# Kernel tuning notes

Measured on AMD Instinct MI355X. Metric: run time of the kernel, lower is better.

Reference implementation:

```python
import jax, jax.numpy as jnp
import numpy as np

B, NS, NN = 1024, 1, 64
F = 128            # feat_dim = edge_dim = time_dim = pos_dim
DM = 4 * F         # model_dim = 512
H, DK = 2, 256     # n_head, d_k = d_v = model_dim // n_head
LN_EPS = 1e-5


def setup_inputs() -> dict:
    key = jax.random.key(0)
    ks = jax.random.split(key, 20)
    s = 0.02
    inp = {
        'src':   jax.random.normal(ks[0], (B, NS, F), jnp.float32),
        'src_t': jax.random.normal(ks[1], (B, NS, F), jnp.float32),
        'src_p': jax.random.normal(ks[2], (B, NS, F), jnp.float32),
        'seq':   jax.random.normal(ks[3], (B, NN, F), jnp.float32),
        'seq_t': jax.random.normal(ks[4], (B, NN, F), jnp.float32),
        'seq_e': jax.random.normal(ks[5], (B, NN, F), jnp.float32),
        'seq_p': jax.random.normal(ks[6], (B, NN, F), jnp.float32),
        'mask':  jax.random.randint(ks[7], (B, NS, NN), 0, 2).astype(bool),
        # MapBasedMultiHeadAttention params
        'wq': jax.random.normal(ks[8], (H * DK, DM), jnp.float32) * s,
        'wk': jax.random.normal(ks[9], (H * DK, DM), jnp.float32) * s,
        'wv': jax.random.normal(ks[10], (H * DK, DM), jnp.float32) * s,
        'wm': jax.random.normal(ks[11], (2 * DK,), jnp.float32) * s,   # weight_map: Linear(2*d_k, 1, bias=False)
        'fc_w': jax.random.normal(ks[12], (DM, H * DK), jnp.float32) * s,
        'fc_b': jnp.zeros((DM,), jnp.float32),
        'ln_g': jnp.ones((DM,), jnp.float32),
        'ln_b': jnp.zeros((DM,), jnp.float32),
        # MergeLayer(model_dim, feat_dim, feat_dim, feat_dim)
        'm1_w': jax.random.normal(ks[13], (F, DM + F), jnp.float32) * s,
        'm1_b': jnp.zeros((F,), jnp.float32),
        'm2_w': jax.random.normal(ks[14], (F, F), jnp.float32) * s,
        'm2_b': jnp.zeros((F,), jnp.float32),
    }
    return inp


def reference(src, src_t, src_p, seq, seq_t, seq_e, seq_p, mask,
              wq, wk, wv, wm, fc_w, fc_b, ln_g, ln_b, m1_w, m1_b, m2_w, m2_b):
    b, ns, f = src.shape
    nn = seq.shape[1]
    src_e = jnp.zeros((b, ns, f), src.dtype)  # edge feats of sources are zero
    q = jnp.concatenate([src, src_e, src_t, src_p], axis=-1)   # [B,NS,DM]
    k = jnp.concatenate([seq, seq_e, seq_t, seq_p], axis=-1)   # [B,NN,DM]

    # per-head projections: weight [H*DK, DM] -> [H, DK, DM]
    qh = jnp.einsum('bsd,hed->bshe', q, wq.reshape(H, DK, DM))  # [B,NS,H,DK]
    kh = jnp.einsum('bnd,hed->bnhe', k, wk.reshape(H, DK, DM))  # [B,NN,H,DK]
    vh = jnp.einsum('bnd,hed->bnhe', k, wv.reshape(H, DK, DM))  # [B,NN,H,DK]

    # weight_map(Linear over concat([q,k])) == q @ wm[:DK] + k @ wm[DK:]
    score_q = jnp.einsum('bshe,e->bhs', qh, wm[:DK])            # [B,H,NS]
    score_k = jnp.einsum('bnhe,e->bhn', kh, wm[DK:])            # [B,H,NN]
    attn = score_q[..., None] + score_k[:, :, None, :]          # [B,H,NS,NN]
    attn = jnp.where(mask[:, None, :, :], jnp.float32(-1e10), attn)
    attn = jax.nn.softmax(attn, axis=-1)

    out = jnp.einsum('bhsn,bnhe->bshe', attn, vh).reshape(b, ns, H * DK)
    out = jnp.einsum('bsd,ed->bse', out, fc_w) + fc_b           # fc
    out = jnp.where(out >= 0, out, 0.2 * out)                   # LeakyReLU(0.2)
    out = out + q                                               # residual
    mu = out.mean(axis=-1, keepdims=True)
    var = out.var(axis=-1, keepdims=True)
    out = (out - mu) / jnp.sqrt(var + LN_EPS) * ln_g + ln_b     # LayerNorm

    # MergeLayer (non_linear=True)
    x = jnp.concatenate([out, src], axis=-1)                    # [B,NS,DM+F]
    hdn = jax.nn.relu(jnp.einsum('bsd,ed->bse', x, m1_w) + m1_b)
    z = jnp.einsum('bsd,ed->bse', hdn, m2_w) + m2_b             # [B,NS,F]

    # attn in original layout: [n_head*B, len_q, len_k]
    attn_flat = attn.transpose(1, 0, 2, 3).reshape(H * b, ns, nn)
    return (z, attn_flat)
```

## Files before the change

kernel.cpp:

```cpp
#include <hip/hip_runtime.h>
#include <hip/hip_bf16.h>
#include <stdint.h>

#define B_   1024
#define NN_  64
#define F_   128
#define DM_  512
#define DK_  256

typedef unsigned short u16;
using f32x4  = __attribute__((ext_vector_type(4))) float;
using bf16x8 = __attribute__((ext_vector_type(8))) short;

__device__ __forceinline__ uint32_t f2bf(float x) {
  uint32_t u = __builtin_bit_cast(uint32_t, x);
  return (u + 0x7fffu + ((u >> 16) & 1u)) >> 16;
}
__device__ __forceinline__ float bf2f(uint32_t us) {
  return __builtin_bit_cast(float, us << 16);
}
__device__ __forceinline__ void split_pack(float x, float y, uint32_t& hp, uint32_t& lp) {
  uint32_t hx = f2bf(x), hy = f2bf(y);
  uint32_t lx = f2bf(x - bf2f(hx)), ly = f2bf(y - bf2f(hy));
  hp = hx | (hy << 16);
  lp = lx | (ly << 16);
}
__device__ __forceinline__ void split1(float x, u16& h, u16& l) {
  uint32_t hx = f2bf(x);
  h = (u16)hx;
  l = (u16)f2bf(x - bf2f(hx));
}

__global__ __launch_bounds__(256) void k_prep(
    const float* __restrict__ wv, const float* __restrict__ fc_w,
    const float* __restrict__ m1_w, const float* __restrict__ m2_w,
    const float* __restrict__ wk, const float* __restrict__ wm,
    u16* __restrict__ fc_hi, u16* __restrict__ fc_lo,
    u16* __restrict__ wvT_hi, u16* __restrict__ wvT_lo,
    u16* __restrict__ m1_hi, u16* __restrict__ m1_lo,
    u16* __restrict__ m2_hi, u16* __restrict__ m2_lo,
    float* __restrict__ wkc) {
  __shared__ float tile[32][33];
  int tid = threadIdx.x;
  int bx = blockIdx.x;

  if (bx >= 256) {
    int t = bx - 256;
    int h = t >> 3, dc = t & 7;
    int w = tid >> 6, l = tid & 63;
    int d = dc * 64 + l;
    const float* base = wk + (size_t)(h * DK_ + w * 64) * DM_ + d;
    float sacc[8] = {0.f, 0.f, 0.f, 0.f, 0.f, 0.f, 0.f, 0.f};
    #pragma unroll
    for (int e = 0; e < 64; ++e)
      sacc[e & 7] += base[e * DM_] * wm[DK_ + w * 64 + e];
    float s = ((sacc[0] + sacc[1]) + (sacc[2] + sacc[3])) +
              ((sacc[4] + sacc[5]) + (sacc[6] + sacc[7]));
    float* part = &tile[0][0];
    part[w * 64 + l] = s;
    __syncthreads();
    if (w == 0)
      wkc[h * DM_ + d] = part[l] + part[64 + l] + part[128 + l] + part[192 + l];
    return;
  }

  int gtid = bx * 256 + tid;
  int nthr = 256 * 256;
  for (int i = gtid; i < DM_ * DM_; i += nthr) split1(fc_w[i], fc_hi[i], fc_lo[i]);
  for (int i = gtid; i < F_ * (DM_ + F_); i += nthr) split1(m1_w[i], m1_hi[i], m1_lo[i]);
  for (int i = gtid; i < F_ * F_; i += nthr) split1(m2_w[i], m2_hi[i], m2_lo[i]);

  int e0 = (bx >> 4) * 32, d0 = (bx & 15) * 32;
  int rr = tid >> 3, c4 = (tid & 7) * 4;
  float4 v = *(const float4*)(wv + (e0 + rr) * DM_ + d0 + c4);
  tile[rr][c4] = v.x; tile[rr][c4 + 1] = v.y;
  tile[rr][c4 + 2] = v.z; tile[rr][c4 + 3] = v.w;
  __syncthreads();
  int dr = tid >> 3, ec = (tid & 7) * 4;
  #pragma unroll
  for (int q = 0; q < 4; ++q) {
    int idx = (d0 + dr) * DM_ + e0 + ec + q;
    split1(tile[ec + q][dr], wvT_hi[idx], wvT_lo[idx]);
  }
}

__device__ __forceinline__ f32x4 mfma_tile_split(
    const u16* __restrict__ Ahi, const u16* __restrict__ Alo, int lda,
    const u16* __restrict__ Bhi, const u16* __restrict__ Blo, int ldb, int K) {
  int l = threadIdx.x & 63;
  int r = l & 15, g = l >> 4;
  int offA = r * lda + g * 8;
  int offB = r * ldb + g * 8;
  f32x4 acc = {0.f, 0.f, 0.f, 0.f};
  for (int k = 0; k < K; k += 32) {
    bf16x8 ah = *(const bf16x8*)(Ahi + offA + k);
    bf16x8 al = *(const bf16x8*)(Alo + offA + k);
    bf16x8 bh = *(const bf16x8*)(Bhi + offB + k);
    bf16x8 bl = *(const bf16x8*)(Blo + offB + k);
    acc = __builtin_amdgcn_mfma_f32_16x16x32_bf16(ah, bh, acc, 0, 0, 0);
    acc = __builtin_amdgcn_mfma_f32_16x16x32_bf16(ah, bl, acc, 0, 0, 0);
    acc = __builtin_amdgcn_mfma_f32_16x16x32_bf16(al, bh, acc, 0, 0, 0);
  }
  return acc;
}

__global__ __launch_bounds__(256) void k_wcomb(
    const u16* __restrict__ fc_hi, const u16* __restrict__ fc_lo,
    const u16* __restrict__ wvT_hi, const u16* __restrict__ wvT_lo,
    u16* __restrict__ wc_hi, u16* __restrict__ wc_lo) {
  int wid = threadIdx.x >> 6;
  int n0g = blockIdx.y * 32;
  int h = n0g >> 9, d0 = n0g & 511;
  int m0 = blockIdx.x * 32 + (wid >> 1) * 16;
  int nb = d0 + (wid & 1) * 16;
  f32x4 acc = mfma_tile_split(fc_hi + m0 * DM_ + h * DK_,
                              fc_lo + m0 * DM_ + h * DK_, DM_,
                              wvT_hi + nb * DM_ + h * DK_,
                              wvT_lo + nb * DM_ + h * DK_, DM_, DK_);
  int l = threadIdx.x & 63, r = l & 15, g = l >> 4;
  #pragma unroll
  for (int i = 0; i < 4; ++i) {
    int m = m0 + g * 4 + i;
    int idx = m * 1024 + n0g + (wid & 1) * 16 + r;
    split1(acc[i], wc_hi[idx], wc_lo[idx]);
  }
}

__global__ __launch_bounds__(256) void k_attn3(
    const float* __restrict__ seq, const float* __restrict__ seq_e,
    const float* __restrict__ seq_t, const float* __restrict__ seq_p,
    const int* __restrict__ mask, const float* __restrict__ wkc,
    float* __restrict__ attn_out,
    uint32_t* __restrict__ kbar_hi, uint32_t* __restrict__ kbar_lo) {
  __shared__ float pbuf[4][64][34];
  __shared__ float els[2][64];
  __shared__ float Zs[2];
  int tid = threadIdx.x, b = blockIdx.x;
  int w = tid >> 6, l = tid & 63;
  int rq = l >> 4, c16 = l & 15;

  const float* arr = (w == 0 ? seq : (w == 1 ? seq_e : (w == 2 ? seq_t : seq_p)));
  const float* base = arr + (size_t)b * 8192 + 8 * c16;
  float c0[8], c1[8];
  #pragma unroll
  for (int u = 0; u < 8; ++u) {
    c0[u] = wkc[w * 128 + 8 * c16 + u];
    c1[u] = wkc[512 + w * 128 + 8 * c16 + u];
  }

  #pragma unroll
  for (int g = 0; g < 4; ++g) {
    float4 va[4], vb[4];
    #pragma unroll
    for (int i = 0; i < 4; ++i) {
      int row = (g * 4 + i) * 4 + rq;
      va[i] = *(const float4*)(base + row * 128);
      vb[i] = *(const float4*)(base + row * 128 + 4);
    }
    #pragma unroll
    for (int i = 0; i < 4; ++i) {
      int row = (g * 4 + i) * 4 + rq;
      float p0 = va[i].x * c0[0] + va[i].y * c0[1] + va[i].z * c0[2] + va[i].w * c0[3]
               + vb[i].x * c0[4] + vb[i].y * c0[5] + vb[i].z * c0[6] + vb[i].w * c0[7];
      float p1 = va[i].x * c1[0] + va[i].y * c1[1] + va[i].z * c1[2] + va[i].w * c1[3]
               + vb[i].x * c1[4] + vb[i].y * c1[5] + vb[i].z * c1[6] + vb[i].w * c1[7];
      float2 t; t.x = p0; t.y = p1;
      *(float2*)&pbuf[w][row][2 * c16] = t;
    }
  }
  __syncthreads();

  if (tid < 128) {
    int h = tid >> 6, row = tid & 63;
    float s = 0.f;
    #pragma unroll
    for (int ww = 0; ww < 4; ++ww)
      #pragma unroll
      for (int c = 0; c < 16; ++c) s += pbuf[ww][row][2 * c + h];
    float e = mask[b * 64 + row] ? 0.f : expf(s);
    els[h][row] = e;
    float z = e;
    #pragma unroll
    for (int off = 32; off; off >>= 1) z += __shfl_xor(z, off);
    attn_out[(h * B_ + b) * 64 + row] = e / z;
    if (row == 0) Zs[h] = z;
  }
  __syncthreads();

  const float* colp = arr + (size_t)b * 8192 + 2 * l;
  float a00 = 0.f, a01 = 0.f, a10 = 0.f, a11 = 0.f;
  #pragma unroll
  for (int jb = 0; jb < 64; jb += 8) {
    float2 v[8];
    #pragma unroll
    for (int u = 0; u < 8; ++u)
      v[u] = *(const float2*)(colp + (jb + u) * 128);
    #pragma unroll
    for (int u = 0; u < 8; ++u) {
      int j = jb + u;
      float t0 = els[0][j], t1 = els[1][j];
      a00 += t0 * v[u].x; a01 += t0 * v[u].y;
      a10 += t1 * v[u].x; a11 += t1 * v[u].y;
    }
  }
  float r0 = 1.f / Zs[0], r1 = 1.f / Zs[1];
  uint32_t hp, lp;
  int idx = b * 512 + tid;
  split_pack(a00 * r0, a01 * r0, hp, lp);
  kbar_hi[idx] = hp; kbar_lo[idx] = lp;
  split_pack(a10 * r1, a11 * r1, hp, lp);
  kbar_hi[idx + 256] = hp; kbar_lo[idx + 256] = lp;
}

__global__ __launch_bounds__(256) void k_fc(
    const u16* __restrict__ kb_hi, const u16* __restrict__ kb_lo,
    const u16* __restrict__ wc_hi, const u16* __restrict__ wc_lo,
    const float* __restrict__ fc_b,
    const float* __restrict__ src, const float* __restrict__ src_t,
    const float* __restrict__ src_p, float* __restrict__ fco) {
  int tid = threadIdx.x;
  int wid = tid >> 6, l = tid & 63;
  int r = l & 15, g = l >> 4;
  int m0 = blockIdx.x * 32 + (wid >> 1) * 16;
  int n0 = blockIdx.y * 64 + (wid & 1) * 32;
  int offA  = (m0 + r) * 1024 + g * 8;
  int offB0 = (n0 + r) * 1024 + g * 8;
  int offB1 = offB0 + 16 * 1024;
  f32x4 acc0 = {0.f, 0.f, 0.f, 0.f}, acc1 = {0.f, 0.f, 0.f, 0.f};
  #pragma unroll 4
  for (int k = 0; k < 1024; k += 32) {
    bf16x8 ah  = *(const bf16x8*)(kb_hi + offA + k);
    bf16x8 al  = *(const bf16x8*)(kb_lo + offA + k);
    bf16x8 b0h = *(const bf16x8*)(wc_hi + offB0 + k);
    bf16x8 b0l = *(const bf16x8*)(wc_lo + offB0 + k);
    bf16x8 b1h = *(const bf16x8*)(wc_hi + offB1 + k);
    bf16x8 b1l = *(const bf16x8*)(wc_lo + offB1 + k);
    acc0 = __builtin_amdgcn_mfma_f32_16x16x32_bf16(ah, b0h, acc0, 0, 0, 0);
    acc0 = __builtin_amdgcn_mfma_f32_16x16x32_bf16(ah, b0l, acc0, 0, 0, 0);
    acc0 = __builtin_amdgcn_mfma_f32_16x16x32_bf16(al, b0h, acc0, 0, 0, 0);
    acc1 = __builtin_amdgcn_mfma_f32_16x16x32_bf16(ah, b1h, acc1, 0, 0, 0);
    acc1 = __builtin_amdgcn_mfma_f32_16x16x32_bf16(ah, b1l, acc1, 0, 0, 0);
    acc1 = __builtin_amdgcn_mfma_f32_16x16x32_bf16(al, b1h, acc1, 0, 0, 0);
  }
  #pragma unroll
  for (int f = 0; f < 2; ++f) {
    int col = n0 + f * 16 + r;
    int part = col >> 7, fc2 = col & 127;
    float bias = fc_b[col];
    const float* qsrc = (part == 0 ? src : (part == 2 ? src_t : src_p));
    #pragma unroll
    for (int i = 0; i < 4; ++i) {
      int m = m0 + g * 4 + i;
      float c = (f == 0 ? acc0[i] : acc1[i]) + bias;
      c = (c >= 0.f) ? c : 0.2f * c;
      float qv = (part == 1) ? 0.f : qsrc[m * 128 + fc2];
      fco[m * 512 + col] = c + qv;
    }
  }
}

__global__ __launch_bounds__(512) void k_m12(
    const float* __restrict__ fco, const float* __restrict__ ln_g,
    const float* __restrict__ ln_b, const float* __restrict__ src,
    const u16* __restrict__ m1_hi, const u16* __restrict__ m1_lo,
    const float* __restrict__ m1_b,
    const u16* __restrict__ m2_hi, const u16* __restrict__ m2_lo,
    const float* __restrict__ m2_b, float* __restrict__ z) {
  __shared__ u16 xh[16][648], xl[16][648];
  __shared__ u16 hh[16][136], hl[16][136];
  int tid = threadIdx.x;
  int m0 = blockIdx.x * 16;

  {
    int row = tid >> 5, l32 = tid & 31;
    int grow = m0 + row;
    float v[16];
    float s = 0.f, s2 = 0.f;
    #pragma unroll
    for (int q = 0; q < 16; ++q) {
      v[q] = fco[grow * 512 + q * 32 + l32];
      s += v[q]; s2 += v[q] * v[q];
    }
    #pragma unroll
    for (int off = 16; off; off >>= 1) {
      s += __shfl_xor(s, off, 32);
      s2 += __shfl_xor(s2, off, 32);
    }
    float mu = s * (1.f / 512.f);
    float var = s2 * (1.f / 512.f) - mu * mu;
    float rstd = rsqrtf(var + 1e-5f);
    #pragma unroll
    for (int q = 0; q < 16; ++q) {
      int col = q * 32 + l32;
      float o = (v[q] - mu) * rstd * ln_g[col] + ln_b[col];
      split1(o, xh[row][col], xl[row][col]);
    }
    #pragma unroll
    for (int q2 = 0; q2 < 4; ++q2) {
      int c = q2 * 32 + l32;
      split1(src[grow * 128 + c], xh[row][512 + c], xl[row][512 + c]);
    }
  }
  __syncthreads();

  int wid = tid >> 6, l = tid & 63;
  int r = l & 15, g = l >> 4;
  int nb = wid * 16;
  {
    f32x4 acc = mfma_tile_split(&xh[0][0], &xl[0][0], 648,
                                m1_hi + nb * 640, m1_lo + nb * 640, 640, 640);
    int col = nb + r;
    float bias = m1_b[col];
    #pragma unroll
    for (int ii = 0; ii < 4; ++ii) {
      int row = g * 4 + ii;
      float o = fmaxf(acc[ii] + bias, 0.f);
      split1(o, hh[row][col], hl[row][col]);
    }
  }
  __syncthreads();
  {
    f32x4 acc = mfma_tile_split(&hh[0][0], &hl[0][0], 136,
                                m2_hi + nb * 128, m2_lo + nb * 128, 128, 128);
    int col = nb + r;
    float bias = m2_b[col];
    #pragma unroll
    for (int ii = 0; ii < 4; ++ii) {
      int row = g * 4 + ii;
      z[(m0 + row) * 128 + col] = acc[ii] + bias;
    }
  }
}

extern "C" void kernel_launch(void* const* d_in, const int* in_sizes, int n_in,
                              void* d_out, int out_size, void* d_ws, size_t ws_size,
                              hipStream_t stream) {
  (void)in_sizes; (void)n_in; (void)out_size; (void)ws_size;
  const float* src   = (const float*)d_in[0];
  const float* src_t = (const float*)d_in[1];
  const float* src_p = (const float*)d_in[2];
  const float* seq   = (const float*)d_in[3];
  const float* seq_t = (const float*)d_in[4];
  const float* seq_e = (const float*)d_in[5];
  const float* seq_p = (const float*)d_in[6];
  const int*   mask  = (const int*)d_in[7];
  const float* wk   = (const float*)d_in[9];
  const float* wv   = (const float*)d_in[10];
  const float* wm   = (const float*)d_in[11];
  const float* fc_w = (const float*)d_in[12];
  const float* fc_b = (const float*)d_in[13];
  const float* ln_g = (const float*)d_in[14];
  const float* ln_b = (const float*)d_in[15];
  const float* m1_w = (const float*)d_in[16];
  const float* m1_b = (const float*)d_in[17];
  const float* m2_w = (const float*)d_in[18];
  const float* m2_b = (const float*)d_in[19];

  float* z_out    = (float*)d_out;
  float* attn_out = z_out + B_ * F_;

  char* ws = (char*)d_ws;
  float* wkc     = (float*)(ws + 0);
  u16* fc_hi     = (u16*)(ws + 4096);
  u16* fc_lo     = (u16*)(ws + 528384);
  u16* m1_hi     = (u16*)(ws + 1052672);
  u16* m1_lo     = (u16*)(ws + 1216512);
  u16* m2_hi     = (u16*)(ws + 1380352);
  u16* m2_lo     = (u16*)(ws + 1413120);
  u16* wvT_hi    = (u16*)(ws + 1445888);
  u16* wvT_lo    = (u16*)(ws + 1970176);
  u16* wc_hi     = (u16*)(ws + 2494464);
  u16* wc_lo     = (u16*)(ws + 3543040);
  uint32_t* kbhi = (uint32_t*)(ws + 4591616);
  uint32_t* kblo = (uint32_t*)(ws + 6688768);
  float* fco     = (float*)(ws + 8785920);

  hipLaunchKernelGGL(k_prep, dim3(272), dim3(256), 0, stream,
                     wv, fc_w, m1_w, m2_w, wk, wm,
                     fc_hi, fc_lo, wvT_hi, wvT_lo,
                     m1_hi, m1_lo, m2_hi, m2_lo, wkc);
  hipLaunchKernelGGL(k_attn3, dim3(1024), dim3(256), 0, stream,
                     seq, seq_e, seq_t, seq_p, mask, wkc,
                     attn_out, kbhi, kblo);
  hipLaunchKernelGGL(k_wcomb, dim3(16, 32), dim3(256), 0, stream,
                     fc_hi, fc_lo, wvT_hi, wvT_lo, wc_hi, wc_lo);
  hipLaunchKernelGGL(k_fc, dim3(32, 8), dim3(256), 0, stream,
                     (const u16*)kbhi, (const u16*)kblo, wc_hi, wc_lo, fc_b,
                     src, src_t, src_p, fco);
  hipLaunchKernelGGL(k_m12, dim3(64), dim3(512), 0, stream,
                     fco, ln_g, ln_b, src,
                     m1_hi, m1_lo, m1_b, m2_hi, m2_lo, m2_b, z_out);
}
```

Baseline: 97.07 us.

## Compute attention scores with bf16 MFMA and reuse K rows staged in LDS

The attention kernel now projects the K rows onto the combined wk·wm vector with bf16 MFMA instructions, using a hi/lo split of the weight vector, in place of scalar FMAs and a cross-warp reduction buffer. The bf16-converted K rows are stored once in a swizzled shared-memory tile. The weighted sum over neighbours then reads from that tile instead of reloading the fp32 inputs from global memory. This cuts the second global read pass but rounds the K features to bf16, which adds precision error to the scores and the pooled output. It also uses about 64KB of LDS per block, which may reduce occupancy.

Measured after the change: 82.62 us. 1.17x faster.

```diff
diff --git a/kernel.cpp b/kernel.cpp
--- a/kernel.cpp
+++ b/kernel.cpp
@@ -126,86 +126,99 @@
   }
 }
 
-__global__ __launch_bounds__(256) void k_attn3(
+__global__ __launch_bounds__(256) void k_attn(
     const float* __restrict__ seq, const float* __restrict__ seq_e,
     const float* __restrict__ seq_t, const float* __restrict__ seq_p,
     const int* __restrict__ mask, const float* __restrict__ wkc,
     float* __restrict__ attn_out,
     uint32_t* __restrict__ kbar_hi, uint32_t* __restrict__ kbar_lo) {
-  __shared__ float pbuf[4][64][34];
+  __shared__ u16 kls[64][512];
+  __shared__ u16 wkb_hi[1024], wkb_lo[1024];
+  __shared__ float sb[2][64];
   __shared__ float els[2][64];
   __shared__ float Zs[2];
+  __shared__ int mlds[64];
   int tid = threadIdx.x, b = blockIdx.x;
-  int w = tid >> 6, l = tid & 63;
-  int rq = l >> 4, c16 = l & 15;
-
-  const float* arr = (w == 0 ? seq : (w == 1 ? seq_e : (w == 2 ? seq_t : seq_p)));
-  const float* base = arr + (size_t)b * 8192 + 8 * c16;
-  float c0[8], c1[8];
+  int ww = tid >> 6, l = tid & 63;
+  int r16 = l & 15, kg = l >> 4;
+
   #pragma unroll
-  for (int u = 0; u < 8; ++u) {
-    c0[u] = wkc[w * 128 + 8 * c16 + u];
-    c1[u] = wkc[512 + w * 128 + 8 * c16 + u];
-  }
-
+  for (int j = 0; j < 4; ++j) {
+    int i = tid * 4 + j;
+    split1(wkc[i], wkb_hi[i], wkb_lo[i]);
+  }
+  if (tid < 64) mlds[tid] = mask[b * 64 + tid];
+  __syncthreads();
+
+  int row = ww * 16 + r16;
+  int rsw = (row & 7);
+  const size_t rb = ((size_t)b * 64 + row) * 128;
+
+  f32x4 acc = {0.f, 0.f, 0.f, 0.f};
   #pragma unroll
-  for (int g = 0; g < 4; ++g) {
+  for (int kk4 = 0; kk4 < 4; ++kk4) {
     float4 va[4], vb[4];
     #pragma unroll
-    for (int i = 0; i < 4; ++i) {
-      int row = (g * 4 + i) * 4 + rq;
-      va[i] = *(const float4*)(base + row * 128);
-      vb[i] = *(const float4*)(base + row * 128 + 4);
-    }
-    #pragma unroll
-    for (int i = 0; i < 4; ++i) {
-      int row = (g * 4 + i) * 4 + rq;
-      float p0 = va[i].x * c0[0] + va[i].y * c0[1] + va[i].z * c0[2] + va[i].w * c0[3]
-               + vb[i].x * c0[4] + vb[i].y * c0[5] + vb[i].z * c0[6] + vb[i].w * c0[7];
-      float p1 = va[i].x * c1[0] + va[i].y * c1[1] + va[i].z * c1[2] + va[i].w * c1[3]
-               + vb[i].x * c1[4] + vb[i].y * c1[5] + vb[i].z * c1[6] + vb[i].w * c1[7];
-      float2 t; t.x = p0; t.y = p1;
-      *(float2*)&pbuf[w][row][2 * c16] = t;
-    }
+    for (int s = 0; s < 4; ++s) {
+      int kk = kk4 * 4 + s;
+      int d = kk * 32 + kg * 8;
+      const float* ap = (d < 128 ? seq : (d < 256 ? seq_e : (d < 384 ? seq_t : seq_p)))
+                        + rb + (d & 127);
+      va[s] = *(const float4*)ap;
+      vb[s] = *(const float4*)(ap + 4);
+    }
+    #pragma unroll
+    for (int s = 0; s < 4; ++s) {
+      int kk = kk4 * 4 + s;
+      int d = kk * 32 + kg * 8;
+      int chunk = d >> 3;
+      bf16x8 kh;
+      kh[0] = (short)f2bf(va[s].x); kh[1] = (short)f2bf(va[s].y);
+      kh[2] = (short)f2bf(va[s].z); kh[3] = (short)f2bf(va[s].w);
+      kh[4] = (short)f2bf(vb[s].x); kh[5] = (short)f2bf(vb[s].y);
+      kh[6] = (short)f2bf(vb[s].z); kh[7] = (short)f2bf(vb[s].w);
+      *(bf16x8*)(&kls[row][(chunk ^ rsw) * 8]) = kh;
+      int wo = (r16 & 1) * 512 + d;
+      bf16x8 wh = *(const bf16x8*)&wkb_hi[wo];
+      bf16x8 wl = *(const bf16x8*)&wkb_lo[wo];
+      acc = __builtin_amdgcn_mfma_f32_16x16x32_bf16(kh, wh, acc, 0, 0, 0);
+      acc = __builtin_amdgcn_mfma_f32_16x16x32_bf16(kh, wl, acc, 0, 0, 0);
+    }
+  }
+  if (r16 < 2) {
+    #pragma unroll
+    for (int i = 0; i < 4; ++i)
+      sb[r16][ww * 16 + kg * 4 + i] = acc[i];
   }
   __syncthreads();
 
   if (tid < 128) {
-    int h = tid >> 6, row = tid & 63;
-    float s = 0.f;
-    #pragma unroll
-    for (int ww = 0; ww < 4; ++ww)
-      #pragma unroll
-      for (int c = 0; c < 16; ++c) s += pbuf[ww][row][2 * c + h];
-    float e = mask[b * 64 + row] ? 0.f : expf(s);
-    els[h][row] = e;
+    int h = tid >> 6, rr = tid & 63;
+    float s = sb[h][rr];
+    float e = mlds[rr] ? 0.f : expf(s);
+    els[h][rr] = e;
     float z = e;
     #pragma unroll
     for (int off = 32; off; off >>= 1) z += __shfl_xor(z, off);
-    attn_out[(h * B_ + b) * 64 + row] = e / z;
-    if (row == 0) Zs[h] = z;
-  }
-  __syncthreads();
-
-  const float* colp = arr + (size_t)b * 8192 + 2 * l;
+    attn_out[(h * B_ + b) * 64 + rr] = e / z;
+    if (rr == 0) Zs[h] = z;
+  }
+  __syncthreads();
+
+  int L = tid;
+  int ch = L >> 2, bo = 2 * (L & 3);
   float a00 = 0.f, a01 = 0.f, a10 = 0.f, a11 = 0.f;
-  #pragma unroll
-  for (int jb = 0; jb < 64; jb += 8) {
-    float2 v[8];
-    #pragma unroll
-    for (int u = 0; u < 8; ++u)
-      v[u] = *(const float2*)(colp + (jb + u) * 128);
-    #pragma unroll
-    for (int u = 0; u < 8; ++u) {
-      int j = jb + u;
-      float t0 = els[0][j], t1 = els[1][j];
-      a00 += t0 * v[u].x; a01 += t0 * v[u].y;
-      a10 += t1 * v[u].x; a11 += t1 * v[u].y;
-    }
+  #pragma unroll 8
+  for (int j = 0; j < 64; ++j) {
+    uint32_t u = *(const uint32_t*)&kls[j][((ch ^ (j & 7))) * 8 + bo];
+    float f0 = bf2f(u & 0xffffu), f1 = bf2f(u >> 16);
+    float e0 = els[0][j], e1 = els[1][j];
+    a00 += e0 * f0; a01 += e0 * f1;
+    a10 += e1 * f0; a11 += e1 * f1;
   }
   float r0 = 1.f / Zs[0], r1 = 1.f / Zs[1];
   uint32_t hp, lp;
-  int idx = b * 512 + tid;
+  int idx = b * 512 + L;
   split_pack(a00 * r0, a01 * r0, hp, lp);
   kbar_hi[idx] = hp; kbar_lo[idx] = lp;
   split_pack(a10 * r1, a11 * r1, hp, lp);
@@ -379,7 +392,7 @@
                      wv, fc_w, m1_w, m2_w, wk, wm,
                      fc_hi, fc_lo, wvT_hi, wvT_lo,
                      m1_hi, m1_lo, m2_hi, m2_lo, wkc);
-  hipLaunchKernelGGL(k_attn3, dim3(1024), dim3(256), 0, stream,
+  hipLaunchKernelGGL(k_attn, dim3(1024), dim3(256), 0, stream,
                      seq, seq_e, seq_t, seq_p, mask, wkc,
                      attn_out, kbhi, kblo);
   hipLaunchKernelGGL(k_wcomb, dim3(16, 32), dim3(256), 0, stream,
```
